# Kernel tuning notes

Hardware: AMD Instinct MI355X
Metric: run time of the kernel (lower is better)

## Reference

```python
import jax, jax.numpy as jnp
import numpy as np

B, T, D, H = 64, 4096, 256, 341  # hidden = 4*256//3 = 341
TAU, RHO, TV_W = 1.0, 0.3, 0.1
NEG = -1e9
EPS = 1e-6
LN_EPS = 1e-5


def entmax15(x, axis=-1):
    """Exact 1.5-entmax via the sort-based threshold algorithm (Peters et al.)."""
    x = (x - jnp.max(x, axis=axis, keepdims=True)) / 2.0
    xsrt = -jnp.sort(-x, axis=axis)                       # descending
    n = x.shape[axis]
    rho = jnp.arange(1, n + 1, dtype=x.dtype)
    mean = jnp.cumsum(xsrt, axis=axis) / rho
    mean_sq = jnp.cumsum(xsrt * xsrt, axis=axis) / rho
    ss = rho * (mean_sq - mean * mean)
    delta = (1.0 - ss) / rho
    tau = mean - jnp.sqrt(jnp.maximum(delta, 0.0))
    support = jnp.sum((tau <= xsrt).astype(jnp.int32), axis=axis, keepdims=True)
    tau_star = jnp.take_along_axis(tau, support - 1, axis=axis)
    return jnp.square(jnp.maximum(x - tau_star, 0.0))


def setup_inputs() -> dict:
    key = jax.random.key(0)
    k_emb, k_len, k_w1, k_w2 = jax.random.split(key, 4)
    embeddings = jax.random.normal(k_emb, (B, T, D), dtype=jnp.float32)
    # variable-length 0/1 attention mask (lengths in [T//4, T]) -> variable k per row
    lengths = jax.random.randint(k_len, (B,), T // 4, T + 1)
    attn = (jnp.arange(T)[None, :] < lengths[:, None]).astype(jnp.float32)
    ln_gamma = jnp.ones((D,), dtype=jnp.float32)
    ln_beta = jnp.zeros((D,), dtype=jnp.float32)
    W1 = jax.random.normal(k_w1, (D, H), dtype=jnp.float32) / np.sqrt(D)
    b1 = jnp.zeros((H,), dtype=jnp.float32)
    W2 = jax.random.normal(k_w2, (H,), dtype=jnp.float32) / np.sqrt(H)
    b2 = jnp.zeros((), dtype=jnp.float32)
    return {"embeddings": embeddings, "attn": attn, "ln_gamma": ln_gamma,
            "ln_beta": ln_beta, "W1": W1, "b1": b1, "W2": W2, "b2": b2}


def reference(embeddings, attn, ln_gamma, ln_beta, W1, b1, W2, b2):
    # SelectorMLP (dropout off at inference)
    emb = embeddings * attn[..., None]                              # [B,T,D]
    mu = jnp.mean(emb, axis=-1, keepdims=True)
    var = jnp.var(emb, axis=-1, keepdims=True)
    xn = (emb - mu) / jnp.sqrt(var + LN_EPS) * ln_gamma + ln_beta
    hid = jax.nn.gelu(jnp.einsum('btd,dh->bth', xn, W1) + b1, approximate=False)
    scores = jnp.einsum('bth,h->bt', hid, W2) + b2                  # [B,T]
    scores = jnp.where(attn == 0, NEG, scores)

    z = entmax15(scores / TAU, axis=1) * attn                       # soft rationale

    # probabilistic_top_k: gumbel-perturbed variable-k top-k, vectorized
    u = jax.random.uniform(jax.random.key(42), scores.shape, dtype=scores.dtype)
    gumbel = -jnp.log(-jnp.log(u + EPS) + EPS)
    pert = scores * attn + gumbel                                   # [B,T]
    t_eff = jnp.sum(attn, axis=1)                                   # [B]
    k = jnp.clip(jnp.round(RHO * t_eff), 1.0, jnp.maximum(t_eff, 1.0)).astype(jnp.int32)
    srt = -jnp.sort(-pert, axis=1)                                  # descending
    thr = jnp.take_along_axis(srt, (k - 1)[:, None], axis=1)        # k-th largest
    h = (pert >= thr).astype(z.dtype) * attn                        # hard mask

    # straight-through estimator
    g = jax.lax.stop_gradient(h - z) + z

    # total variation regularizer on g within valid region
    dz = jnp.abs(g[:, 1:] - g[:, :-1])
    valid = attn[:, 1:] * attn[:, :-1]
    tv = jnp.mean(jnp.sum(dz * valid, axis=1) / jnp.maximum(jnp.sum(valid, axis=1), 1.0))
    reg = TV_W * tv
    return (z, g, reg)
```

## Files before the change

### kernel.cpp

```cpp
#include <hip/hip_runtime.h>
#include <stdint.h>

#define BB 64
#define TT 4096
#define DD 256
#define HH 341
#define HP 384
#define NEGV (-1e9f)

typedef __attribute__((ext_vector_type(8))) short short8;
typedef __attribute__((ext_vector_type(4))) float f32x4;


__device__ inline float gelu_fast(float x) {
  const float y = fabsf(x) * 0.70710678118654752440f;
  const float t = __builtin_amdgcn_rcpf(fmaf(0.3275911f, y, 1.0f));
  float p = fmaf(1.061405429f, t, -1.453152027f);
  p = fmaf(p, t, 1.421413741f);
  p = fmaf(p, t, -0.284496736f);
  p = fmaf(p, t, 0.254829592f);
  p *= t;
  const float e = __expf(-y * y);
  float er = fmaf(-p, e, 1.0f);
  er = (x < 0.0f) ? -er : er;
  return 0.5f * x * (1.0f + er);
}

__device__ inline uint32_t rotl32(uint32_t x, int d) { return (x << d) | (x >> (32 - d)); }

__device__ inline uint32_t threefry_bits(uint32_t j) {
  const uint32_t K0 = 0u, K1 = 42u;
  const uint32_t K2 = K0 ^ K1 ^ 0x1BD11BDAu;
  uint32_t x0 = 0u, x1 = j;
  x0 += K0; x1 += K1;
#define TF_RND(r) { x0 += x1; x1 = rotl32(x1, r); x1 ^= x0; }
  TF_RND(13) TF_RND(15) TF_RND(26) TF_RND(6)
  x0 += K1; x1 += K2 + 1u;
  TF_RND(17) TF_RND(29) TF_RND(16) TF_RND(24)
  x0 += K2; x1 += K0 + 2u;
  TF_RND(13) TF_RND(15) TF_RND(26) TF_RND(6)
  x0 += K0; x1 += K1 + 3u;
  TF_RND(17) TF_RND(29) TF_RND(16) TF_RND(24)
  x0 += K1; x1 += K2 + 4u;
  TF_RND(13) TF_RND(15) TF_RND(26) TF_RND(6)
  x0 += K2; x1 += K0 + 5u;
#undef TF_RND
  return x0 ^ x1;
}

__device__ inline void bf16split(float x, short& hi, short& lo) {
  uint32_t u = __float_as_uint(x);
  uint32_t h = (u + 0x7FFFu + ((u >> 16) & 1u)) >> 16;
  float rem = x - __uint_as_float(h << 16);
  uint32_t ur = __float_as_uint(rem);
  uint32_t l = (ur + 0x7FFFu + ((ur >> 16) & 1u)) >> 16;
  hi = (short)h; lo = (short)l;
}

__device__ inline float bred_sum(float v, volatile float* tmp, int tid) {
#pragma unroll
  for (int o = 32; o; o >>= 1) v += __shfl_xor(v, o, 64);
  __syncthreads();
  if ((tid & 63) == 0) tmp[tid >> 6] = v;
  __syncthreads();
  return tmp[0] + tmp[1] + tmp[2] + tmp[3];
}

__device__ inline float bred_max(float v, volatile float* tmp, int tid) {
#pragma unroll
  for (int o = 32; o; o >>= 1) v = fmaxf(v, __shfl_xor(v, o, 64));
  __syncthreads();
  if ((tid & 63) == 0) tmp[tid >> 6] = v;
  __syncthreads();
  return fmaxf(fmaxf(tmp[0], tmp[1]), fmaxf(tmp[2], tmp[3]));
}

__device__ inline void bred_sum2(float& a, float& b, volatile float* tmp, int tid) {
#pragma unroll
  for (int o = 32; o; o >>= 1) { a += __shfl_xor(a, o, 64); b += __shfl_xor(b, o, 64); }
  __syncthreads();
  if ((tid & 63) == 0) { int w2 = (tid >> 6) * 2; tmp[w2] = a; tmp[w2 + 1] = b; }
  __syncthreads();
  a = tmp[0] + tmp[2] + tmp[4] + tmp[6];
  b = tmp[1] + tmp[3] + tmp[5] + tmp[7];
}

__device__ inline void bred3_i(int& a, int& b, int& c, volatile int* tmp, int tid) {
#pragma unroll
  for (int o = 32; o; o >>= 1) {
    a += __shfl_xor(a, o, 64);
    b += __shfl_xor(b, o, 64);
    c += __shfl_xor(c, o, 64);
  }
  __syncthreads();
  if ((tid & 63) == 0) { int w3 = (tid >> 6) * 3; tmp[w3] = a; tmp[w3 + 1] = b; tmp[w3 + 2] = c; }
  __syncthreads();
  a = tmp[0] + tmp[3] + tmp[6] + tmp[9];
  b = tmp[1] + tmp[4] + tmp[7] + tmp[10];
  c = tmp[2] + tmp[5] + tmp[8] + tmp[11];
}


__global__ __launch_bounds__(256) void k0_prep(const float* __restrict__ W1,
                                               short* __restrict__ Whi,
                                               short* __restrict__ Wlo) {
  int idx = blockIdx.x * 256 + threadIdx.x;
  int h = idx >> 8, k = idx & 255;
  float v = (h < HH) ? W1[k * HH + h] : 0.0f;
  short hi, lo;
  bf16split(v, hi, lo);
  Whi[idx] = hi;
  Wlo[idx] = lo;
}


__global__ __launch_bounds__(512, 4) void k1_mfma(
    const float* __restrict__ emb, const float* __restrict__ attn,
    const float* __restrict__ gamma, const float* __restrict__ beta,
    const short* __restrict__ Whi, const float* __restrict__ b1,
    const float* __restrict__ W2, const float* __restrict__ b2,
    float* __restrict__ scores) {
  __shared__ short Ahi[16384];
  __shared__ short Alo[16384];

  const int bid = blockIdx.x;
  const int b = bid >> 6;
  const int t0 = (bid & 63) * 64;
  const int tid = threadIdx.x;
  const int w = tid >> 6;
  const int lane = tid & 63;

  if (attn[(size_t)b * TT + t0] == 0.0f) {
    if (tid < 64) scores[(size_t)b * TT + t0 + tid] = NEGV;
    return;
  }

  {
    const int half = lane >> 5;
    const int g = lane & 31;
    const int k0g = g >> 2, qg = g & 3;
    float gg[8], bb[8];
#pragma unroll
    for (int j = 0; j < 8; ++j) { gg[j] = gamma[g * 8 + j]; bb[j] = beta[g * 8 + j]; }

    for (int it = 0; it < 4; ++it) {
      const int il = w * 8 + it * 2 + half;
      const size_t rowoff = (size_t)b * TT + t0 + il;
      const float a = attn[rowoff];
      const float* ep = emb + rowoff * DD + g * 8;
      float x[8];
      {
        float4 xA = *(const float4*)ep;
        float4 xB = *(const float4*)(ep + 4);
        x[0] = xA.x * a; x[1] = xA.y * a; x[2] = xA.z * a; x[3] = xA.w * a;
        x[4] = xB.x * a; x[5] = xB.y * a; x[6] = xB.z * a; x[7] = xB.w * a;
      }
      float s = 0.f, ss = 0.f;
#pragma unroll
      for (int j = 0; j < 8; ++j) { s += x[j]; ss += x[j] * x[j]; }
#pragma unroll
      for (int o = 16; o; o >>= 1) { s += __shfl_xor(s, o, 32); ss += __shfl_xor(ss, o, 32); }
      const float mu = s * (1.0f / DD);
      const float rs = 1.0f / sqrtf(ss * (1.0f / DD) - mu * mu + 1e-5f);

      short8 h8, l8;
#pragma unroll
      for (int j = 0; j < 8; ++j) {
        float y = (x[j] - mu) * rs * gg[j] + bb[j];
        short hi, lo;
        bf16split(y, hi, lo);
        h8[j] = hi; l8[j] = lo;
      }
      const int i15 = il & 15, mt = il >> 4;
      const int slot = mt * 512 + k0g * 64 + qg * 16 + (i15 ^ k0g);
      *(short8*)&Ahi[slot * 8] = h8;
      *(short8*)&Alo[slot * 8] = l8;
    }
  }
  __syncthreads();

  const int r = lane & 15, q = lane >> 4;
  f32x4 acc[3][4];
#pragma unroll
  for (int j = 0; j < 3; ++j)
#pragma unroll
    for (int mt = 0; mt < 4; ++mt) acc[j][mt] = (f32x4){0.f, 0.f, 0.f, 0.f};

  int hb[3];
#pragma unroll
  for (int j = 0; j < 3; ++j) hb[j] = ((w * 3 + j) * 16 + r) * 256 + q * 8;

  for (int k0 = 0; k0 < 8; ++k0) {
    short8 ahi[4], alo[4];
#pragma unroll
    for (int mt = 0; mt < 4; ++mt) {
      const int slot = mt * 512 + k0 * 64 + q * 16 + (r ^ k0);
      ahi[mt] = *(const short8*)&Ahi[slot * 8];
      alo[mt] = *(const short8*)&Alo[slot * 8];
    }
#pragma unroll
    for (int j = 0; j < 3; ++j) {
      const short* bp = Whi + hb[j] + k0 * 32;
      short8 bhi = *(const short8*)bp;
      short8 blo = *(const short8*)(bp + HP * DD);
#pragma unroll
      for (int mt = 0; mt < 4; ++mt) {
        acc[j][mt] = __builtin_amdgcn_mfma_f32_16x16x32_bf16(ahi[mt], bhi, acc[j][mt], 0, 0, 0);
        acc[j][mt] = __builtin_amdgcn_mfma_f32_16x16x32_bf16(ahi[mt], blo, acc[j][mt], 0, 0, 0);
        acc[j][mt] = __builtin_amdgcn_mfma_f32_16x16x32_bf16(alo[mt], bhi, acc[j][mt], 0, 0, 0);
      }
    }
  }

  float part[4][4];
#pragma unroll
  for (int mt = 0; mt < 4; ++mt)
#pragma unroll
    for (int rr = 0; rr < 4; ++rr) part[mt][rr] = 0.f;

#pragma unroll
  for (int j = 0; j < 3; ++j) {
    const int h = (w * 3 + j) * 16 + r;
    const float w2v = (h < HH) ? W2[h] : 0.f;
    const float b1v = (h < HH) ? b1[h] : 0.f;
#pragma unroll
    for (int mt = 0; mt < 4; ++mt)
#pragma unroll
      for (int rr = 0; rr < 4; ++rr)
        part[mt][rr] += gelu_fast(acc[j][mt][rr] + b1v) * w2v;
  }

  float sacc[4][4];
#pragma unroll
  for (int mt = 0; mt < 4; ++mt)
#pragma unroll
    for (int rr = 0; rr < 4; ++rr) {
      float v = part[mt][rr];
      v += __shfl_xor(v, 1, 64);
      v += __shfl_xor(v, 2, 64);
      v += __shfl_xor(v, 4, 64);
      v += __shfl_xor(v, 8, 64);
      sacc[mt][rr] = v;
    }

  __syncthreads();
  float* sred = (float*)Ahi;
  if (r == 0) {
#pragma unroll
    for (int mt = 0; mt < 4; ++mt)
#pragma unroll
      for (int rr = 0; rr < 4; ++rr)
        sred[w * 64 + mt * 16 + q * 4 + rr] = sacc[mt][rr];
  }
  __syncthreads();

  if (tid < 64) {
    float sc = b2[0];
#pragma unroll
    for (int ww = 0; ww < 8; ++ww) sc += sred[ww * 64 + tid];
    float a = attn[(size_t)b * TT + t0 + tid];
    scores[(size_t)b * TT + t0 + tid] = (a != 0.f) ? sc : NEGV;
  }
}


__global__ __launch_bounds__(256) void k2_select(
    const float* __restrict__ attn, float* __restrict__ out, float* __restrict__ row_tv) {
  __shared__ float gs[TT];
  __shared__ float ftmp[8];
  __shared__ int itmp[12];

  const int b = blockIdx.x, tid = threadIdx.x;
  const float* arow = attn + (size_t)b * TT;
  float* zrow = out + (size_t)b * TT;
  float* grow = out + (size_t)BB * TT + (size_t)b * TT;

  float x_loc[16], a_loc[16];
  uint32_t key_loc[16];
  float cnt = 0.0f, mx = -3.4e38f;
#pragma unroll
  for (int i = 0; i < 16; ++i) {
    int t = tid + i * 256;
    float s = grow[t];
    float a = arow[t];
    a_loc[i] = a;
    x_loc[i] = s;
    cnt += a;
    mx = fmaxf(mx, s);
    uint32_t bits = threefry_bits((uint32_t)(b * TT + t));
    float u = __uint_as_float(0x3F800000u | (bits >> 9)) - 1.0f;
    float gum = -logf(1e-6f - logf(u + 1e-6f));
    float pert = (a != 0.0f ? s : 0.0f) + gum;
    uint32_t fb = __float_as_uint(pert);
    uint32_t msk = ((int32_t)fb < 0) ? 0xFFFFFFFFu : 0x80000000u;
    key_loc[i] = fb ^ msk;
  }
  float t_eff = bred_sum(cnt, ftmp, tid);
  mx = bred_max(mx, ftmp, tid);

#pragma unroll
  for (int i = 0; i < 16; ++i) x_loc[i] = (x_loc[i] - mx) * 0.5f;

  float tau = -1.0f;
  for (int it = 0; it < 18; ++it) {
    float f = 0.0f, g = 0.0f;
#pragma unroll
    for (int i = 0; i < 16; ++i) {
      float d = x_loc[i] - tau;
      if (d > 0.0f) { f = fmaf(d, d, f); g += d; }
    }
    bred_sum2(f, g, ftmp, tid);
    tau = fminf(tau + (f - 1.0f) / (2.0f * g), -0.015625f);
  }

  float kf = rintf(0.3f * t_eff);
  kf = fminf(fmaxf(kf, 1.0f), fmaxf(t_eff, 1.0f));
  int kk = (int)kf;

  uint32_t prefix = 0u;
  for (int bit = 30; bit >= 0; bit -= 2) {
    uint32_t ph = (prefix >> 2) >> bit;
    int c1 = 0, c2 = 0, c3 = 0;
#pragma unroll
    for (int i = 0; i < 16; ++i) {
      uint32_t kb = key_loc[i];
      bool m = (((kb >> 2) >> bit) == ph);
      uint32_t d = (kb >> bit) & 3u;
      c1 += (int)(m && d >= 1u);
      c2 += (int)(m && d >= 2u);
      c3 += (int)(m && d == 3u);
    }
    bred3_i(c1, c2, c3, itmp, tid);
    uint32_t dig;
    if (c3 >= kk) dig = 3u;
    else if (c2 >= kk) { dig = 2u; kk -= c3; }
    else if (c1 >= kk) { dig = 1u; kk -= c2; }
    else { dig = 0u; kk -= c1; }
    prefix |= dig << bit;
  }
  const uint32_t thr = prefix;

#pragma unroll
  for (int i = 0; i < 16; ++i) {
    int t = tid + i * 256;
    float d = x_loc[i] - tau;
    float z = (d > 0.0f) ? d * d : 0.0f;
    z *= a_loc[i];
    float h = (key_loc[i] >= thr) ? a_loc[i] : 0.0f;
    float g = (h - z) + z;
    zrow[t] = z;
    gs[t] = g;
  }
  __syncthreads();

  float tvn = 0.0f, tvd = 0.0f;
#pragma unroll
  for (int i = 0; i < 16; ++i) {
    int t = tid + i * 256;
    grow[t] = gs[t];
    if (t > 0) {
      float valid = arow[t] * arow[t - 1];
      tvn += fabsf(gs[t] - gs[t - 1]) * valid;
      tvd += valid;
    }
  }
  tvn = bred_sum(tvn, ftmp, tid);
  tvd = bred_sum(tvd, ftmp, tid);
  if (tid == 0) row_tv[b] = tvn / fmaxf(tvd, 1.0f);
}


__global__ __launch_bounds__(64) void k3_final(const float* __restrict__ row_tv,
                                               float* __restrict__ out) {
  float v = row_tv[threadIdx.x];
#pragma unroll
  for (int o = 32; o; o >>= 1) v += __shfl_xor(v, o, 64);
  if (threadIdx.x == 0) out[2 * BB * TT] = 0.1f * (v * (1.0f / BB));
}


extern "C" void kernel_launch(void* const* d_in, const int* in_sizes, int n_in,
                              void* d_out, int out_size, void* d_ws, size_t ws_size,
                              hipStream_t stream) {
  const float* emb   = (const float*)d_in[0];
  const float* attn  = (const float*)d_in[1];
  const float* gamma = (const float*)d_in[2];
  const float* beta  = (const float*)d_in[3];
  const float* W1    = (const float*)d_in[4];
  const float* b1    = (const float*)d_in[5];
  const float* W2    = (const float*)d_in[6];
  const float* b2    = (const float*)d_in[7];
  float* out = (float*)d_out;

  float* row_tv = (float*)d_ws;
  short* Whi = (short*)((char*)d_ws + 512);
  short* Wlo = Whi + HP * DD;

  k0_prep<<<dim3(HP * DD / 256), dim3(256), 0, stream>>>(W1, Whi, Wlo);
  k1_mfma<<<dim3(BB * TT / 64), dim3(512), 0, stream>>>(
      emb, attn, gamma, beta, Whi, b1, W2, b2, out + (size_t)BB * TT);
  k2_select<<<dim3(BB), dim3(256), 0, stream>>>(attn, out, row_tv);
  k3_final<<<dim3(1), dim3(64), 0, stream>>>(row_tv, out);
}
```

Measured before the change: 553.6 us.

## Halve k1 row tile, drop final kernel via last-block atomic, fuse reductions

The MFMA scoring kernel now processes 32 tokens per block instead of 64. This halves LDS and accumulator registers and doubles the grid, with launch bounds raised to 6 blocks per CU to improve occupancy and load balance. Embedding loads are batched before the LayerNorm math, and the k0 prep kernel is reorganised so W1 reads are coalesced. The separate final-reduction kernel is removed: the last k2 block, found with an atomic counter, sums the per-row TV values. Sum and max reductions in k2 are fused to save a barrier pair. The cost is more weight (B-operand) traffic per token, since each W tile is reused across fewer rows.

```diff
diff --git a/kernel.cpp b/kernel.cpp
--- a/kernel.cpp
+++ b/kernel.cpp
@@ -66,13 +66,14 @@
   return tmp[0] + tmp[1] + tmp[2] + tmp[3];
 }
 
-__device__ inline float bred_max(float v, volatile float* tmp, int tid) {
-#pragma unroll
-  for (int o = 32; o; o >>= 1) v = fmaxf(v, __shfl_xor(v, o, 64));
-  __syncthreads();
-  if ((tid & 63) == 0) tmp[tid >> 6] = v;
-  __syncthreads();
-  return fmaxf(fmaxf(tmp[0], tmp[1]), fmaxf(tmp[2], tmp[3]));
+__device__ inline void bred_summax(float& a, float& b, volatile float* tmp, int tid) {
+#pragma unroll
+  for (int o = 32; o; o >>= 1) { a += __shfl_xor(a, o, 64); b = fmaxf(b, __shfl_xor(b, o, 64)); }
+  __syncthreads();
+  if ((tid & 63) == 0) { int w2 = (tid >> 6) * 2; tmp[w2] = a; tmp[w2 + 1] = b; }
+  __syncthreads();
+  a = tmp[0] + tmp[2] + tmp[4] + tmp[6];
+  b = fmaxf(fmaxf(tmp[1], tmp[3]), fmaxf(tmp[5], tmp[7]));
 }
 
 __device__ inline void bred_sum2(float& a, float& b, volatile float* tmp, int tid) {
@@ -101,37 +102,39 @@
 }
 
 
-__global__ __launch_bounds__(256) void k0_prep(const float* __restrict__ W1,
+__global__ __launch_bounds__(384) void k0_prep(const float* __restrict__ W1,
                                                short* __restrict__ Whi,
-                                               short* __restrict__ Wlo) {
-  int idx = blockIdx.x * 256 + threadIdx.x;
-  int h = idx >> 8, k = idx & 255;
+                                               short* __restrict__ Wlo,
+                                               int* __restrict__ done_ctr) {
+  const int k = blockIdx.x;
+  const int h = threadIdx.x;
+  if (k == 0 && h == 0) *done_ctr = 0;
   float v = (h < HH) ? W1[k * HH + h] : 0.0f;
   short hi, lo;
   bf16split(v, hi, lo);
-  Whi[idx] = hi;
-  Wlo[idx] = lo;
-}
-
-
-__global__ __launch_bounds__(512, 4) void k1_mfma(
+  Whi[h * DD + k] = hi;
+  Wlo[h * DD + k] = lo;
+}
+
+
+__global__ __launch_bounds__(512, 6) void k1_mfma(
     const float* __restrict__ emb, const float* __restrict__ attn,
     const float* __restrict__ gamma, const float* __restrict__ beta,
     const short* __restrict__ Whi, const float* __restrict__ b1,
     const float* __restrict__ W2, const float* __restrict__ b2,
     float* __restrict__ scores) {
-  __shared__ short Ahi[16384];
-  __shared__ short Alo[16384];
+  __shared__ short Ahi[8192];
+  __shared__ short Alo[8192];
 
   const int bid = blockIdx.x;
-  const int b = bid >> 6;
-  const int t0 = (bid & 63) * 64;
+  const int b = bid >> 7;
+  const int t0 = (bid & 127) * 32;
   const int tid = threadIdx.x;
   const int w = tid >> 6;
   const int lane = tid & 63;
 
   if (attn[(size_t)b * TT + t0] == 0.0f) {
-    if (tid < 64) scores[(size_t)b * TT + t0 + tid] = NEGV;
+    if (tid < 32) scores[(size_t)b * TT + t0 + tid] = NEGV;
     return;
   }
 
@@ -143,18 +146,25 @@
 #pragma unroll
     for (int j = 0; j < 8; ++j) { gg[j] = gamma[g * 8 + j]; bb[j] = beta[g * 8 + j]; }
 
-    for (int it = 0; it < 4; ++it) {
-      const int il = w * 8 + it * 2 + half;
+    float a2[2];
+    float4 xA2[2], xB2[2];
+#pragma unroll
+    for (int it = 0; it < 2; ++it) {
+      const int il = w * 4 + it * 2 + half;
       const size_t rowoff = (size_t)b * TT + t0 + il;
-      const float a = attn[rowoff];
+      a2[it] = attn[rowoff];
       const float* ep = emb + rowoff * DD + g * 8;
+      xA2[it] = *(const float4*)ep;
+      xB2[it] = *(const float4*)(ep + 4);
+    }
+
+#pragma unroll
+    for (int it = 0; it < 2; ++it) {
+      const int il = w * 4 + it * 2 + half;
+      const float a = a2[it];
       float x[8];
-      {
-        float4 xA = *(const float4*)ep;
-        float4 xB = *(const float4*)(ep + 4);
-        x[0] = xA.x * a; x[1] = xA.y * a; x[2] = xA.z * a; x[3] = xA.w * a;
-        x[4] = xB.x * a; x[5] = xB.y * a; x[6] = xB.z * a; x[7] = xB.w * a;
-      }
+      x[0] = xA2[it].x * a; x[1] = xA2[it].y * a; x[2] = xA2[it].z * a; x[3] = xA2[it].w * a;
+      x[4] = xB2[it].x * a; x[5] = xB2[it].y * a; x[6] = xB2[it].z * a; x[7] = xB2[it].w * a;
       float s = 0.f, ss = 0.f;
 #pragma unroll
       for (int j = 0; j < 8; ++j) { s += x[j]; ss += x[j] * x[j]; }
@@ -180,20 +190,21 @@
   __syncthreads();
 
   const int r = lane & 15, q = lane >> 4;
-  f32x4 acc[3][4];
+  f32x4 acc[3][2];
 #pragma unroll
   for (int j = 0; j < 3; ++j)
 #pragma unroll
-    for (int mt = 0; mt < 4; ++mt) acc[j][mt] = (f32x4){0.f, 0.f, 0.f, 0.f};
+    for (int mt = 0; mt < 2; ++mt) acc[j][mt] = (f32x4){0.f, 0.f, 0.f, 0.f};
 
   int hb[3];
 #pragma unroll
   for (int j = 0; j < 3; ++j) hb[j] = ((w * 3 + j) * 16 + r) * 256 + q * 8;
 
+#pragma unroll
   for (int k0 = 0; k0 < 8; ++k0) {
-    short8 ahi[4], alo[4];
-#pragma unroll
-    for (int mt = 0; mt < 4; ++mt) {
+    short8 ahi[2], alo[2];
+#pragma unroll
+    for (int mt = 0; mt < 2; ++mt) {
       const int slot = mt * 512 + k0 * 64 + q * 16 + (r ^ k0);
       ahi[mt] = *(const short8*)&Ahi[slot * 8];
       alo[mt] = *(const short8*)&Alo[slot * 8];
@@ -204,7 +215,7 @@
       short8 bhi = *(const short8*)bp;
       short8 blo = *(const short8*)(bp + HP * DD);
 #pragma unroll
-      for (int mt = 0; mt < 4; ++mt) {
+      for (int mt = 0; mt < 2; ++mt) {
         acc[j][mt] = __builtin_amdgcn_mfma_f32_16x16x32_bf16(ahi[mt], bhi, acc[j][mt], 0, 0, 0);
         acc[j][mt] = __builtin_amdgcn_mfma_f32_16x16x32_bf16(ahi[mt], blo, acc[j][mt], 0, 0, 0);
         acc[j][mt] = __builtin_amdgcn_mfma_f32_16x16x32_bf16(alo[mt], bhi, acc[j][mt], 0, 0, 0);
@@ -212,9 +223,9 @@
     }
   }
 
-  float part[4][4];
-#pragma unroll
-  for (int mt = 0; mt < 4; ++mt)
+  float part[2][4];
+#pragma unroll
+  for (int mt = 0; mt < 2; ++mt)
 #pragma unroll
     for (int rr = 0; rr < 4; ++rr) part[mt][rr] = 0.f;
 
@@ -224,15 +235,15 @@
     const float w2v = (h < HH) ? W2[h] : 0.f;
     const float b1v = (h < HH) ? b1[h] : 0.f;
 #pragma unroll
-    for (int mt = 0; mt < 4; ++mt)
+    for (int mt = 0; mt < 2; ++mt)
 #pragma unroll
       for (int rr = 0; rr < 4; ++rr)
         part[mt][rr] += gelu_fast(acc[j][mt][rr] + b1v) * w2v;
   }
 
-  float sacc[4][4];
-#pragma unroll
-  for (int mt = 0; mt < 4; ++mt)
+  float sacc[2][4];
+#pragma unroll
+  for (int mt = 0; mt < 2; ++mt)
 #pragma unroll
     for (int rr = 0; rr < 4; ++rr) {
       float v = part[mt][rr];
@@ -247,17 +258,17 @@
   float* sred = (float*)Ahi;
   if (r == 0) {
 #pragma unroll
-    for (int mt = 0; mt < 4; ++mt)
+    for (int mt = 0; mt < 2; ++mt)
 #pragma unroll
       for (int rr = 0; rr < 4; ++rr)
-        sred[w * 64 + mt * 16 + q * 4 + rr] = sacc[mt][rr];
-  }
-  __syncthreads();
-
-  if (tid < 64) {
+        sred[w * 32 + mt * 16 + q * 4 + rr] = sacc[mt][rr];
+  }
+  __syncthreads();
+
+  if (tid < 32) {
     float sc = b2[0];
 #pragma unroll
-    for (int ww = 0; ww < 8; ++ww) sc += sred[ww * 64 + tid];
+    for (int ww = 0; ww < 8; ++ww) sc += sred[ww * 32 + tid];
     float a = attn[(size_t)b * TT + t0 + tid];
     scores[(size_t)b * TT + t0 + tid] = (a != 0.f) ? sc : NEGV;
   }
@@ -265,10 +276,12 @@
 
 
 __global__ __launch_bounds__(256) void k2_select(
-    const float* __restrict__ attn, float* __restrict__ out, float* __restrict__ row_tv) {
+    const float* __restrict__ attn, float* __restrict__ out,
+    float* __restrict__ row_tv, int* __restrict__ done_ctr) {
   __shared__ float gs[TT];
   __shared__ float ftmp[8];
   __shared__ int itmp[12];
+  __shared__ int is_last;
 
   const int b = blockIdx.x, tid = threadIdx.x;
   const float* arow = attn + (size_t)b * TT;
@@ -295,8 +308,8 @@
     uint32_t msk = ((int32_t)fb < 0) ? 0xFFFFFFFFu : 0x80000000u;
     key_loc[i] = fb ^ msk;
   }
-  float t_eff = bred_sum(cnt, ftmp, tid);
-  mx = bred_max(mx, ftmp, tid);
+  float t_eff = cnt;
+  bred_summax(t_eff, mx, ftmp, tid);
 
 #pragma unroll
   for (int i = 0; i < 16; ++i) x_loc[i] = (x_loc[i] - mx) * 0.5f;
@@ -366,16 +379,22 @@
   }
   tvn = bred_sum(tvn, ftmp, tid);
   tvd = bred_sum(tvd, ftmp, tid);
-  if (tid == 0) row_tv[b] = tvn / fmaxf(tvd, 1.0f);
-}
-
-
-__global__ __launch_bounds__(64) void k3_final(const float* __restrict__ row_tv,
-                                               float* __restrict__ out) {
-  float v = row_tv[threadIdx.x];
-#pragma unroll
-  for (int o = 32; o; o >>= 1) v += __shfl_xor(v, o, 64);
-  if (threadIdx.x == 0) out[2 * BB * TT] = 0.1f * (v * (1.0f / BB));
+
+  if (tid == 0) {
+    __hip_atomic_store(&row_tv[b], tvn / fmaxf(tvd, 1.0f),
+                       __ATOMIC_RELEASE, __HIP_MEMORY_SCOPE_AGENT);
+    int prev = __hip_atomic_fetch_add(done_ctr, 1,
+                                      __ATOMIC_ACQ_REL, __HIP_MEMORY_SCOPE_AGENT);
+    is_last = (prev == BB - 1) ? 1 : 0;
+  }
+  __syncthreads();
+  if (is_last && tid < 64) {
+    float v = __hip_atomic_load(&row_tv[tid],
+                                __ATOMIC_ACQUIRE, __HIP_MEMORY_SCOPE_AGENT);
+#pragma unroll
+    for (int o = 32; o; o >>= 1) v += __shfl_xor(v, o, 64);
+    if (tid == 0) out[2 * BB * TT] = 0.1f * (v * (1.0f / BB));
+  }
 }
 
 
@@ -393,12 +412,12 @@
   float* out = (float*)d_out;
 
   float* row_tv = (float*)d_ws;
+  int* done_ctr = (int*)((char*)d_ws + 256);
   short* Whi = (short*)((char*)d_ws + 512);
   short* Wlo = Whi + HP * DD;
 
-  k0_prep<<<dim3(HP * DD / 256), dim3(256), 0, stream>>>(W1, Whi, Wlo);
-  k1_mfma<<<dim3(BB * TT / 64), dim3(512), 0, stream>>>(
+  k0_prep<<<dim3(DD), dim3(HP), 0, stream>>>(W1, Whi, Wlo, done_ctr);
+  k1_mfma<<<dim3(BB * TT / 32), dim3(512), 0, stream>>>(
       emb, attn, gamma, beta, Whi, b1, W2, b2, out + (size_t)BB * TT);
-  k2_select<<<dim3(BB), dim3(256), 0, stream>>>(attn, out, row_tv);
-  k3_final<<<dim3(1), dim3(64), 0, stream>>>(row_tv, out);
-}
+  k2_select<<<dim3(BB), dim3(256), 0, stream>>>(attn, out, row_tv, done_ctr);
+}
```

New measurement: 616.7 us. 1.11x slower.
